# Kernel optimization log

Measured on AMD Instinct MI355X. Metric: run time of the kernel, lower is better.

Reference implementation:

```python
import jax, jax.numpy as jnp
import numpy as np

EMBED = 768
HEADS = 12
HEAD_DIM = EMBED // HEADS  # 64


def setup_inputs() -> dict:
    key = jax.random.key(0)
    ks = jax.random.split(key, 9)
    d = HEAD_DIM
    s = 1.0 / np.sqrt(d)
    return {
        "x": jax.random.normal(ks[0], (8, 1024, EMBED), dtype=jnp.float32),
        "ln_w": jnp.ones((EMBED,), dtype=jnp.float32),
        "ln_b": jnp.zeros((EMBED,), dtype=jnp.float32),
        "Wq": jax.random.uniform(ks[1], (d, d), jnp.float32, -s, s),
        "bq": jax.random.uniform(ks[2], (d,), jnp.float32, -s, s),
        "Wk": jax.random.uniform(ks[3], (d, d), jnp.float32, -s, s),
        "bk": jax.random.uniform(ks[4], (d,), jnp.float32, -s, s),
        "Wv": jax.random.uniform(ks[5], (d, d), jnp.float32, -s, s),
        "bv": jax.random.uniform(ks[6], (d,), jnp.float32, -s, s),
    }


def reference(x, ln_w, ln_b, Wq, bq, Wk, bk, Wv, bv):
    bs, n, e = x.shape
    # LayerNorm over last dim (eps matches torch default 1e-5)
    mu = jnp.mean(x, axis=-1, keepdims=True)
    var = jnp.mean(jnp.square(x - mu), axis=-1, keepdims=True)
    xn = (x - mu) / jnp.sqrt(var + 1e-5) * ln_w + ln_b
    # Raw view split (NOT transpose split): [bs, n, E] -> [bs, H, n, d]
    xh = xn.reshape(bs, HEADS, n, HEAD_DIM)
    # Linear layers (torch Linear: y = x @ W.T + b)
    q = jnp.einsum("bhnd,ed->bhne", xh, Wq) + bq
    k = jnp.einsum("bhnd,ed->bhne", xh, Wk) + bk
    v = jnp.einsum("bhnd,ed->bhne", xh, Wv) + bv
    # Unusual: softmax FIRST, then divide by sqrt(d)
    scores = jnp.einsum("bhqd,bhkd->bhqk", q, k)
    attn = jax.nn.softmax(scores, axis=-1) / jnp.sqrt(jnp.float32(HEAD_DIM))
    feature = jnp.einsum("bhqk,bhkd->bhqd", attn, v)
    return feature.reshape(bs, n, e)
```

## Files before the change

### kernel.cpp

```cpp
#include <hip/hip_runtime.h>

#define EMBED 768
#define HEADS 12
#define HD 64
#define SEQ 1024
#define BS 8
#define NROWS (BS * HEADS * SEQ)
#define XP 72
#define PLP 40
#define LOG2E 1.4426950408889634f

typedef _Float16 f16;
typedef f16 f16x4 __attribute__((ext_vector_type(4)));
typedef f16 f16x8 __attribute__((ext_vector_type(8)));
typedef float f32x4 __attribute__((ext_vector_type(4)));

__global__ __launch_bounds__(256) void k_lnstats(const float* __restrict__ x,
                                                 const float* __restrict__ Wq,
                                                 const float* __restrict__ Wk,
                                                 const float* __restrict__ Wv,
                                                 float* __restrict__ mu_out,
                                                 float* __restrict__ rs_out,
                                                 f16* __restrict__ wf) {
    const int w = threadIdx.x >> 6;
    const int lane = threadIdx.x & 63;
    const int row = blockIdx.x * 4 + w;
    const float4* xr = (const float4*)(x + (long)row * EMBED);
    float s = 0.f, sq = 0.f;
#pragma unroll
    for (int kk = 0; kk < 3; ++kk) {
        float4 v = xr[lane + kk * 64];
        s += v.x + v.y + v.z + v.w;
        sq += v.x * v.x + v.y * v.y + v.z * v.z + v.w * v.w;
    }
#pragma unroll
    for (int off = 32; off; off >>= 1) {
        s += __shfl_xor(s, off, 64);
        sq += __shfl_xor(sq, off, 64);
    }
    if (lane == 0) {
        float mu = s * (1.f / EMBED);
        float var = sq * (1.f / EMBED) - mu * mu;
        mu_out[row] = mu;
        rs_out[row] = rsqrtf(var + 1e-5f);
    }
    if (blockIdx.x < 3) {
        const float* W = (blockIdx.x == 0) ? Wq : (blockIdx.x == 1) ? Wk : Wv;
        const float sc = (blockIdx.x == 0) ? LOG2E : 1.0f;
        f16* dst = wf + (long)blockIdx.x * 4096;
        const int t = threadIdx.x;
#pragma unroll
        for (int i = 0; i < 2; ++i) {
            const int o = t * 2 + i;
            const int nt = o >> 7, half = (o >> 6) & 1, lp = o & 63;
            const int qd = lp >> 4, l16 = lp & 15;
            const float* src = W + (nt * 16 + l16) * 64 + half * 32 + qd * 8;
            float4 v0 = *(const float4*)src, v1 = *(const float4*)(src + 4);
            f16x8 h = {(f16)(v0.x * sc), (f16)(v0.y * sc), (f16)(v0.z * sc), (f16)(v0.w * sc),
                       (f16)(v1.x * sc), (f16)(v1.y * sc), (f16)(v1.z * sc), (f16)(v1.w * sc)};
            *(f16x8*)(dst + o * 8) = h;
        }
    }
}

__global__ __launch_bounds__(256) void k_qkv(
    const float* __restrict__ x, const float* __restrict__ lw, const float* __restrict__ lb,
    const f16* __restrict__ wf,
    const float* __restrict__ bq, const float* __restrict__ bk, const float* __restrict__ bv,
    const float* __restrict__ mu, const float* __restrict__ rs,
    f16* __restrict__ qo, f16* __restrict__ ko, f16* __restrict__ vo) {
    __shared__ __align__(16) f16 xh[2][64 * XP];
    __shared__ __align__(16) f16 kb[2][4096];
    __shared__ __align__(16) f16 vb[2][4096];
    const int t = threadIdx.x;
    const unsigned r0 = (unsigned)blockIdx.x * 128;
    const int bh = (int)(r0 >> 10);
    const int seq0 = (int)(r0 & 1023);
    const int tile0 = seq0 >> 5;

#pragma unroll
    for (int st = 0; st < 2; ++st) {
        const unsigned fb = (r0 + st * 64u) * 64u + (unsigned)t * 16u;
        const unsigned xrow = fb / EMBED;
        const unsigned c0 = fb % EMBED;
        const float m_ = mu[xrow], s_ = rs[xrow];
        const int lrow = (t * 16) >> 6, lcol = (t * 16) & 63;
        f16* dst = &xh[st][lrow * XP + lcol];
        const float4* xp = (const float4*)(x + fb);
        const float4* wp = (const float4*)(lw + c0);
        const float4* bp = (const float4*)(lb + c0);
#pragma unroll
        for (int j = 0; j < 4; ++j) {
            float4 xv = xp[j], wv = wp[j], bv2 = bp[j];
            f16x4 h = {(f16)((xv.x - m_) * s_ * wv.x + bv2.x), (f16)((xv.y - m_) * s_ * wv.y + bv2.y),
                       (f16)((xv.z - m_) * s_ * wv.z + bv2.z), (f16)((xv.w - m_) * s_ * wv.w + bv2.w)};
            *(f16x4*)(dst + j * 4) = h;
        }
    }

    const int lane = t & 63, w = t >> 6, l16 = lane & 15, quad = lane >> 4;
    f16x8 a[2][2];
#pragma unroll
    for (int st = 0; st < 2; ++st) {
        a[st][0] = *(const f16x8*)&xh[st][(w * 16 + l16) * XP + quad * 8];
        a[st][1] = *(const f16x8*)&xh[st][(w * 16 + l16) * XP + 32 + quad * 8];
    }
    const float* Bs[3] = {bq, bk, bv};

#pragma unroll
    for (int m = 0; m < 3; ++m) {
        const f16* wfm = wf + (long)m * 4096 + lane * 8;
        const float bsc = (m == 0) ? LOG2E : 1.0f;
        f32x4 acc[2][4];
#pragma unroll
        for (int nt = 0; nt < 4; ++nt) {
            f16x8 b0 = *(const f16x8*)(wfm + (nt * 2 + 0) * 512);
            f16x8 b1 = *(const f16x8*)(wfm + (nt * 2 + 1) * 512);
            const float bias = Bs[m][nt * 16 + l16] * bsc;
#pragma unroll
            for (int st = 0; st < 2; ++st) {
                f32x4 a_ = {0.f, 0.f, 0.f, 0.f};
                a_ = __builtin_amdgcn_mfma_f32_16x16x32_f16(a[st][0], b0, a_, 0, 0, 0);
                a_ = __builtin_amdgcn_mfma_f32_16x16x32_f16(a[st][1], b1, a_, 0, 0, 0);
#pragma unroll
                for (int rg = 0; rg < 4; ++rg) a_[rg] += bias;
                acc[st][nt] = a_;
            }
        }
        if (m == 0) {
#pragma unroll
            for (int st = 0; st < 2; ++st)
#pragma unroll
                for (int nt = 0; nt < 4; ++nt)
#pragma unroll
                    for (int rg = 0; rg < 4; ++rg)
                        xh[st][(w * 16 + quad * 4 + rg) * XP + nt * 16 + l16] = (f16)acc[st][nt][rg];
        } else if (m == 1) {
#pragma unroll
            for (int st = 0; st < 2; ++st)
#pragma unroll
                for (int nt = 0; nt < 4; ++nt) {
                    const int base = (w >> 1) * 2048 + ((w & 1) * 2 + (nt >> 1)) * 512 +
                                     ((((nt & 1) << 1) | (l16 >> 3))) * 128 + (quad * 4) * 8 + (l16 & 7);
#pragma unroll
                    for (int rg = 0; rg < 4; ++rg)
                        kb[st][base + rg * 8] = (f16)acc[st][nt][rg];
                }
        } else {
#pragma unroll
            for (int st = 0; st < 2; ++st)
#pragma unroll
                for (int nt = 0; nt < 4; ++nt) {
                    const int base = (w >> 1) * 2048 + nt * 512 + quad * 128 + l16 * 8 + (w & 1);
#pragma unroll
                    for (int rg = 0; rg < 4; ++rg)
                        vb[st][base + rg * 2] = (f16)acc[st][nt][rg];
                }
        }
    }

    __syncthreads();

#pragma unroll
    for (int st = 0; st < 2; ++st)
#pragma unroll
        for (int c = t; c < 512; c += 256) {
            const int row = c >> 3, c8 = (c & 7) * 8;
            *(f16x8*)(qo + ((long)r0 + st * 64 + row) * 64 + c8) = *(const f16x8*)&xh[st][row * XP + c8];
        }
    {
        f16* kg = ko + ((long)bh << 16) + (long)tile0 * 2048;
        f16* vg = vo + ((long)bh << 16) + (long)tile0 * 2048;
        const f16* kfl = &kb[0][0];
        const f16* vfl = &vb[0][0];
#pragma unroll
        for (int i = 0; i < 4; ++i) {
            const int o = (t + i * 256) * 8;
            *(f16x8*)(kg + o) = *(const f16x8*)(kfl + o);
            *(f16x8*)(vg + o) = *(const f16x8*)(vfl + o);
        }
    }
}

__global__ __launch_bounds__(256) void k_attn(const f16* __restrict__ q,
                                              const f16* __restrict__ k,
                                              const f16* __restrict__ vt,
                                              float* __restrict__ out) {
    __shared__ __align__(16) f16 pl[4][32 * PLP];
    const int t = threadIdx.x;
    const int w = t >> 6, lane = t & 63, l16 = lane & 15, quad = lane >> 4;
    const int bh = blockIdx.x;
    const int q0 = blockIdx.y * 128 + w * 32;
    const long hb = (long)bh * SEQ;
    const f16* kp0 = k + ((long)bh << 16) + lane * 8;
    const f16* vp0 = vt + ((long)bh << 16) + lane * 8;

    f16x8 qf[2][2];
#pragma unroll
    for (int mt = 0; mt < 2; ++mt) {
        const f16* qp = q + (hb + q0 + mt * 16 + l16) * 64 + quad * 8;
        qf[mt][0] = *(const f16x8*)qp;
        qf[mt][1] = *(const f16x8*)(qp + 32);
    }
    f32x4 o[2][4];
    f32x4 ls[2];
#pragma unroll
    for (int mt = 0; mt < 2; ++mt) {
        ls[mt] = (f32x4){0.f, 0.f, 0.f, 0.f};
#pragma unroll
        for (int nt = 0; nt < 4; ++nt) o[mt][nt] = (f32x4){0.f, 0.f, 0.f, 0.f};
    }
    f16x8 one;
#pragma unroll
    for (int j = 0; j < 8; ++j) one[j] = (f16)1.0f;
    const float C0 = -14.f * LOG2E;
    const f32x4 cinit = {C0, C0, C0, C0};

#define LOADK(kt, kf)                                  \
    {                                                  \
        const f16* kp = kp0 + (kt) * 2048;             \
        kf[0] = *(const f16x8*)kp;                     \
        kf[1] = *(const f16x8*)(kp + 512);             \
        kf[2] = *(const f16x8*)(kp + 1024);            \
        kf[3] = *(const f16x8*)(kp + 1536);            \
    }
#define LOADV(kt, vf)                                  \
    {                                                  \
        const f16* vp = vp0 + (kt) * 2048;             \
        vf[0] = *(const f16x8*)vp;                     \
        vf[1] = *(const f16x8*)(vp + 512);             \
        vf[2] = *(const f16x8*)(vp + 1024);            \
        vf[3] = *(const f16x8*)(vp + 1536);            \
    }

    f16x8 ka[4], va[4], kb[4], vb[4];
    LOADK(0, ka);
    LOADV(0, va);

    auto body = [&](const f16x8* kf, const f16x8* vf) {
        f32x4 s[2][2];
#pragma unroll
        for (int mt = 0; mt < 2; ++mt) {
            f32x4 a = cinit;
            a = __builtin_amdgcn_mfma_f32_16x16x32_f16(qf[mt][0], kf[0], a, 0, 0, 0);
            a = __builtin_amdgcn_mfma_f32_16x16x32_f16(qf[mt][1], kf[1], a, 0, 0, 0);
            s[mt][0] = a;
            f32x4 b = cinit;
            b = __builtin_amdgcn_mfma_f32_16x16x32_f16(qf[mt][0], kf[2], b, 0, 0, 0);
            b = __builtin_amdgcn_mfma_f32_16x16x32_f16(qf[mt][1], kf[3], b, 0, 0, 0);
            s[mt][1] = b;
        }
#pragma unroll
        for (int mt = 0; mt < 2; ++mt)
#pragma unroll
            for (int rg = 0; rg < 4; ++rg) {
                float e0, e1;
                asm("v_exp_f32 %0, %1" : "=v"(e0) : "v"(s[mt][0][rg]));
                asm("v_exp_f32 %0, %1" : "=v"(e1) : "v"(s[mt][1][rg]));
                auto pk = __builtin_amdgcn_cvt_pkrtz(e0, e1);
                *(decltype(pk)*)&pl[w][(mt * 16 + quad * 4 + rg) * PLP + l16 * 2] = pk;
            }
        f16x8 pf0 = *(const f16x8*)&pl[w][l16 * PLP + quad * 8];
        f16x8 pf1 = *(const f16x8*)&pl[w][(16 + l16) * PLP + quad * 8];
        ls[0] = __builtin_amdgcn_mfma_f32_16x16x32_f16(pf0, one, ls[0], 0, 0, 0);
        ls[1] = __builtin_amdgcn_mfma_f32_16x16x32_f16(pf1, one, ls[1], 0, 0, 0);
#pragma unroll
        for (int nt = 0; nt < 4; ++nt) {
            o[0][nt] = __builtin_amdgcn_mfma_f32_16x16x32_f16(pf0, vf[nt], o[0][nt], 0, 0, 0);
            o[1][nt] = __builtin_amdgcn_mfma_f32_16x16x32_f16(pf1, vf[nt], o[1][nt], 0, 0, 0);
        }
    };

    for (int kt = 0; kt < SEQ / 32; kt += 2) {
        LOADK(kt + 1, kb);
        LOADV(kt + 1, vb);
        body(ka, va);
        const int kn = (kt + 2 < SEQ / 32) ? kt + 2 : SEQ / 32 - 1;
        LOADK(kn, ka);
        LOADV(kn, va);
        body(kb, vb);
    }
#undef LOADK
#undef LOADV

#pragma unroll
    for (int mt = 0; mt < 2; ++mt) {
        float inv[4];
#pragma unroll
        for (int rg = 0; rg < 4; ++rg) inv[rg] = 1.f / (ls[mt][rg] * 8.0f);
#pragma unroll
        for (int nt = 0; nt < 4; ++nt) {
            float* op = out + (hb + q0 + mt * 16 + quad * 4) * 64 + nt * 16 + l16;
#pragma unroll
            for (int rg = 0; rg < 4; ++rg) op[(long)rg * 64] = o[mt][nt][rg] * inv[rg];
        }
    }
}

extern "C" void kernel_launch(void* const* d_in, const int* in_sizes, int n_in,
                              void* d_out, int out_size, void* d_ws, size_t ws_size,
                              hipStream_t stream) {
    const float* x = (const float*)d_in[0];
    const float* lw = (const float*)d_in[1];
    const float* lb = (const float*)d_in[2];
    const float* Wq = (const float*)d_in[3];
    const float* bq = (const float*)d_in[4];
    const float* Wk = (const float*)d_in[5];
    const float* bk = (const float*)d_in[6];
    const float* Wv = (const float*)d_in[7];
    const float* bv = (const float*)d_in[8];
    float* out = (float*)d_out;

    char* ws = (char*)d_ws;
    float* mu = (float*)ws;
    float* rs = (float*)(ws + 32768);
    f16* wfr = (f16*)(ws + 65536);
    f16* qo = (f16*)(ws + 98304);
    f16* ko = qo + (long)NROWS * 64;
    f16* vo = ko + (long)NROWS * 64;

    k_lnstats<<<2048, 256, 0, stream>>>(x, Wq, Wk, Wv, mu, rs, wfr);
    k_qkv<<<NROWS / 128, 256, 0, stream>>>(x, lw, lb, wfr, bq, bk, bv, mu, rs, qo, ko, vo);
    k_attn<<<dim3(BS * HEADS, SEQ / 128), 256, 0, stream>>>(qo, ko, vo, out);
}
```

Measured before the change: 137.1 us.

## Fuse LayerNorm statistics into QKV projection kernel, drop separate stats pass

Moves the per-row mean and rstd computation out of a standalone 2048-block kernel and into the QKV projection kernel. Each block computes stats for the up to 12 input rows its tile spans and keeps them in shared memory. Weight conversion is now a tiny 3-block kernel. This removes a full extra pass over x and the mu/rs round trip, at the cost of x rows being read twice inside k_qkv (L2-resident) and an added barrier.

```diff
diff --git a/kernel.cpp b/kernel.cpp
--- a/kernel.cpp
+++ b/kernel.cpp
@@ -15,51 +15,24 @@
 typedef f16 f16x8 __attribute__((ext_vector_type(8)));
 typedef float f32x4 __attribute__((ext_vector_type(4)));
 
-__global__ __launch_bounds__(256) void k_lnstats(const float* __restrict__ x,
-                                                 const float* __restrict__ Wq,
-                                                 const float* __restrict__ Wk,
-                                                 const float* __restrict__ Wv,
-                                                 float* __restrict__ mu_out,
-                                                 float* __restrict__ rs_out,
-                                                 f16* __restrict__ wf) {
-    const int w = threadIdx.x >> 6;
-    const int lane = threadIdx.x & 63;
-    const int row = blockIdx.x * 4 + w;
-    const float4* xr = (const float4*)(x + (long)row * EMBED);
-    float s = 0.f, sq = 0.f;
-#pragma unroll
-    for (int kk = 0; kk < 3; ++kk) {
-        float4 v = xr[lane + kk * 64];
-        s += v.x + v.y + v.z + v.w;
-        sq += v.x * v.x + v.y * v.y + v.z * v.z + v.w * v.w;
-    }
-#pragma unroll
-    for (int off = 32; off; off >>= 1) {
-        s += __shfl_xor(s, off, 64);
-        sq += __shfl_xor(sq, off, 64);
-    }
-    if (lane == 0) {
-        float mu = s * (1.f / EMBED);
-        float var = sq * (1.f / EMBED) - mu * mu;
-        mu_out[row] = mu;
-        rs_out[row] = rsqrtf(var + 1e-5f);
-    }
-    if (blockIdx.x < 3) {
-        const float* W = (blockIdx.x == 0) ? Wq : (blockIdx.x == 1) ? Wk : Wv;
-        const float sc = (blockIdx.x == 0) ? LOG2E : 1.0f;
-        f16* dst = wf + (long)blockIdx.x * 4096;
-        const int t = threadIdx.x;
-#pragma unroll
-        for (int i = 0; i < 2; ++i) {
-            const int o = t * 2 + i;
-            const int nt = o >> 7, half = (o >> 6) & 1, lp = o & 63;
-            const int qd = lp >> 4, l16 = lp & 15;
-            const float* src = W + (nt * 16 + l16) * 64 + half * 32 + qd * 8;
-            float4 v0 = *(const float4*)src, v1 = *(const float4*)(src + 4);
-            f16x8 h = {(f16)(v0.x * sc), (f16)(v0.y * sc), (f16)(v0.z * sc), (f16)(v0.w * sc),
-                       (f16)(v1.x * sc), (f16)(v1.y * sc), (f16)(v1.z * sc), (f16)(v1.w * sc)};
-            *(f16x8*)(dst + o * 8) = h;
-        }
+__global__ __launch_bounds__(256) void k_wconv(const float* __restrict__ Wq,
+                                               const float* __restrict__ Wk,
+                                               const float* __restrict__ Wv,
+                                               f16* __restrict__ wf) {
+    const float* W = (blockIdx.x == 0) ? Wq : (blockIdx.x == 1) ? Wk : Wv;
+    const float sc = (blockIdx.x == 0) ? LOG2E : 1.0f;
+    f16* dst = wf + (long)blockIdx.x * 4096;
+    const int t = threadIdx.x;
+#pragma unroll
+    for (int i = 0; i < 2; ++i) {
+        const int o = t * 2 + i;
+        const int nt = o >> 7, half = (o >> 6) & 1, lp = o & 63;
+        const int qd = lp >> 4, l16 = lp & 15;
+        const float* src = W + (nt * 16 + l16) * 64 + half * 32 + qd * 8;
+        float4 v0 = *(const float4*)src, v1 = *(const float4*)(src + 4);
+        f16x8 h = {(f16)(v0.x * sc), (f16)(v0.y * sc), (f16)(v0.z * sc), (f16)(v0.w * sc),
+                   (f16)(v1.x * sc), (f16)(v1.y * sc), (f16)(v1.z * sc), (f16)(v1.w * sc)};
+        *(f16x8*)(dst + o * 8) = h;
     }
 }
 
@@ -67,23 +40,50 @@
     const float* __restrict__ x, const float* __restrict__ lw, const float* __restrict__ lb,
     const f16* __restrict__ wf,
     const float* __restrict__ bq, const float* __restrict__ bk, const float* __restrict__ bv,
-    const float* __restrict__ mu, const float* __restrict__ rs,
     f16* __restrict__ qo, f16* __restrict__ ko, f16* __restrict__ vo) {
     __shared__ __align__(16) f16 xh[2][64 * XP];
     __shared__ __align__(16) f16 kb[2][4096];
     __shared__ __align__(16) f16 vb[2][4096];
+    __shared__ float smu[12], srs[12];
     const int t = threadIdx.x;
     const unsigned r0 = (unsigned)blockIdx.x * 128;
     const int bh = (int)(r0 >> 10);
     const int seq0 = (int)(r0 & 1023);
     const int tile0 = seq0 >> 5;
+    const int lane = t & 63, w = t >> 6, l16 = lane & 15, quad = lane >> 4;
+
+    const unsigned fb0 = r0 * 64u;
+    const int xr0 = (int)(fb0 / EMBED);
+    const int xrN = (int)((fb0 + 8191u) / EMBED) - xr0 + 1;
+    for (int ri = w; ri < xrN; ri += 4) {
+        const float4* xr_ = (const float4*)(x + (long)(xr0 + ri) * EMBED);
+        float s = 0.f, sq = 0.f;
+#pragma unroll
+        for (int kk = 0; kk < 3; ++kk) {
+            float4 v = xr_[lane + kk * 64];
+            s += v.x + v.y + v.z + v.w;
+            sq += v.x * v.x + v.y * v.y + v.z * v.z + v.w * v.w;
+        }
+#pragma unroll
+        for (int off = 32; off; off >>= 1) {
+            s += __shfl_xor(s, off, 64);
+            sq += __shfl_xor(sq, off, 64);
+        }
+        if (lane == 0) {
+            float mu = s * (1.f / EMBED);
+            float var = sq * (1.f / EMBED) - mu * mu;
+            smu[ri] = mu;
+            srs[ri] = rsqrtf(var + 1e-5f);
+        }
+    }
+    __syncthreads();
 
 #pragma unroll
     for (int st = 0; st < 2; ++st) {
-        const unsigned fb = (r0 + st * 64u) * 64u + (unsigned)t * 16u;
+        const unsigned fb = fb0 + st * 4096u + (unsigned)t * 16u;
         const unsigned xrow = fb / EMBED;
         const unsigned c0 = fb % EMBED;
-        const float m_ = mu[xrow], s_ = rs[xrow];
+        const float m_ = smu[xrow - xr0], s_ = srs[xrow - xr0];
         const int lrow = (t * 16) >> 6, lcol = (t * 16) & 63;
         f16* dst = &xh[st][lrow * XP + lcol];
         const float4* xp = (const float4*)(x + fb);
@@ -98,7 +98,6 @@
         }
     }
 
-    const int lane = t & 63, w = t >> 6, l16 = lane & 15, quad = lane >> 4;
     f16x8 a[2][2];
 #pragma unroll
     for (int st = 0; st < 2; ++st) {
@@ -312,14 +311,12 @@
     float* out = (float*)d_out;
 
     char* ws = (char*)d_ws;
-    float* mu = (float*)ws;
-    float* rs = (float*)(ws + 32768);
-    f16* wfr = (f16*)(ws + 65536);
-    f16* qo = (f16*)(ws + 98304);
+    f16* wfr = (f16*)ws;
+    f16* qo = (f16*)(ws + 32768);
     f16* ko = qo + (long)NROWS * 64;
     f16* vo = ko + (long)NROWS * 64;
 
-    k_lnstats<<<2048, 256, 0, stream>>>(x, Wq, Wk, Wv, mu, rs, wfr);
-    k_qkv<<<NROWS / 128, 256, 0, stream>>>(x, lw, lb, wfr, bq, bk, bv, mu, rs, qo, ko, vo);
+    k_wconv<<<3, 256, 0, stream>>>(Wq, Wk, Wv, wfr);
+    k_qkv<<<NROWS / 128, 256, 0, stream>>>(x, lw, lb, wfr, bq, bk, bv, qo, ko, vo);
     k_attn<<<dim3(BS * HEADS, SEQ / 128), 256, 0, stream>>>(qo, ko, vo, out);
 }
```

Result: no change. 138.7 us (+1.2%).
